# Kernel tuning notes

Measured on AMD Instinct MI355X. Metric: run time of the kernel, lower is better.

Reference implementation:

```python
import jax, jax.numpy as jnp
import numpy as np

N = 10000
E = 80000
NUM_TYPES = 1000
IN_CH = 64
EMB = 128
IN_GNN = EMB + IN_CH - 1  # 191
NUM_GRAPHS = 16
NUM_CLASSES = 2


def _glorot(key, shape):
    fan_in, fan_out = shape[0], shape[1]
    lim = jnp.sqrt(6.0 / (fan_in + fan_out))
    return jax.random.uniform(key, shape, jnp.float32, -lim, lim)


def setup_inputs() -> dict:
    key = jax.random.key(0)
    ks = jax.random.split(key, 20)
    node_type_ids = jax.random.randint(ks[0], (N,), 0, NUM_TYPES)
    other_feats = jax.random.normal(ks[1], (N, IN_CH - 1), jnp.float32)
    edge_index = jax.random.randint(ks[2], (2, E), 0, N)
    batch = jnp.sort(jax.random.randint(ks[3], (N,), 0, NUM_GRAPHS))
    params = dict(
        emb=jax.random.normal(ks[4], (NUM_TYPES, EMB), jnp.float32),
        W1=_glorot(ks[5], (IN_GNN, 2048)), b1=jnp.zeros((2048,), jnp.float32),
        W2=_glorot(ks[6], (2048, 1024)), b2=jnp.zeros((1024,), jnp.float32),
        W3=_glorot(ks[7], (1024, 1024)), b3=jnp.zeros((1024,), jnp.float32),
        h1w=_glorot(ks[8], (1024, 1024)), h1b=jnp.zeros((1024,), jnp.float32),
        h2w=_glorot(ks[9], (1024, 1024)), h2b=jnp.zeros((1024,), jnp.float32),
        h3w=_glorot(ks[10], (1024, 512)), h3b=jnp.zeros((512,), jnp.float32),
        ow=_glorot(ks[11], (512, NUM_CLASSES)), ob=jnp.zeros((NUM_CLASSES,), jnp.float32),
    )
    return dict(node_type_ids=node_type_ids, other_feats=other_feats,
                edge_index=edge_index, batch=batch, **params)


def _gcn_norm(edge_index, num_nodes):
    # add self loops + symmetric normalization D^-1/2 (A+I) D^-1/2 (PyG GCNConv defaults)
    loop = jnp.arange(num_nodes, dtype=edge_index.dtype)
    src = jnp.concatenate([edge_index[0], loop])
    dst = jnp.concatenate([edge_index[1], loop])
    deg = jax.ops.segment_sum(jnp.ones_like(src, jnp.float32), dst, num_segments=num_nodes)
    dinv = jnp.where(deg > 0, jax.lax.rsqrt(jnp.maximum(deg, 1.0)), 0.0)
    norm = dinv[src] * dinv[dst]
    return src, dst, norm


def _gcn_conv(x, src, dst, norm, W, b):
    h = x @ W                                    # [N, out] dense GEMM first (PyG order)
    msg = h[src] * norm[:, None]                 # gather + scale over edges
    agg = jax.ops.segment_sum(msg, dst, num_segments=x.shape[0])  # scatter-add
    return agg + b


def reference(node_type_ids, other_feats, edge_index, batch,
              emb, W1, b1, W2, b2, W3, b3,
              h1w, h1b, h2w, h2b, h3w, h3b, ow, ob):
    # eval mode: dropout is identity
    x = jnp.concatenate([emb[node_type_ids], other_feats], axis=-1)  # [N, 191]
    src, dst, norm = _gcn_norm(edge_index, x.shape[0])
    x = jax.nn.relu(_gcn_conv(x, src, dst, norm, W1, b1))
    x = jax.nn.relu(_gcn_conv(x, src, dst, norm, W2, b2))
    x = jax.nn.relu(_gcn_conv(x, src, dst, norm, W3, b3))
    # global mean pool over graphs
    sums = jax.ops.segment_sum(x, batch, num_segments=NUM_GRAPHS)
    cnts = jax.ops.segment_sum(jnp.ones((x.shape[0],), jnp.float32), batch, num_segments=NUM_GRAPHS)
    g = sums / jnp.maximum(cnts, 1.0)[:, None]   # [G, 1024]
    g = jax.nn.relu(g @ h1w + h1b)
    g = jax.nn.relu(g @ h2w + h2b)
    g = jax.nn.relu(g @ h3w + h3b)
    return g @ ow + ob                           # [G, num_classes]
```

## Files before the change

kernel.cpp:

```cpp
#include <hip/hip_runtime.h>


#define N_NODES 10000
#define N_EDGES 80000
#define EMB_DIM 128
#define FEAT_DIM 63
#define IN_GNN 191
#define IN_STRIDE 192
#define H1 2048
#define H2 1024
#define NGRAPH 16
#define NCLS 2
#define PCHUNK 8

using ushort = unsigned short;
typedef __attribute__((ext_vector_type(8))) short s8b;
typedef __attribute__((ext_vector_type(4))) float f4v;

__device__ __forceinline__ float us2f(ushort u) {
    union { unsigned int i; float f; } v; v.i = ((unsigned int)u) << 16; return v.f;
}
__device__ __forceinline__ ushort f2us(float f) {
    union { unsigned int i; float f; } v; v.f = f;
    unsigned int r = v.i + 0x7FFFu + ((v.i >> 16) & 1u);
    return (ushort)(r >> 16);
}
__device__ __forceinline__ float ldm(const void* p, long i, int md) {
    return (md == 1) ? us2f(((const ushort*)p)[i]) : ((const float*)p)[i];
}

__global__ void GraphV1EmbLarge_73864847556672_kernel() {}

__global__ void k_prep0(int* __restrict__ a, int na, float* __restrict__ b, int nb,
                        const ushort* __restrict__ feats, int* __restrict__ mode) {
    int i = blockIdx.x * 256 + threadIdx.x;
    if (i < na) a[i] = 0;
    if (i < nb) b[i] = 0.f;
    if (blockIdx.x == 0 && threadIdx.x == 0) {
        int sane = 0;
        for (int j = 0; j < 256; j++) {
            ushort u = feats[j];
            int e = (u >> 7) & 0xFF;
            if (u == 0 || (e >= 97 && e <= 157)) sane++;
        }
        *mode = (sane >= 220) ? 1 : 2;
    }
}

__global__ void k_deg_i(const int* __restrict__ dst, int* __restrict__ cnt) {
    int e = blockIdx.x * blockDim.x + threadIdx.x;
    if (e < N_EDGES) atomicAdd(&cnt[dst[e]], 1);
}
__global__ void k_scan(const int* __restrict__ cnt, int* __restrict__ indptr,
                       float* __restrict__ dinv) {
    __shared__ int part[256];
    int t = threadIdx.x;
    int base = t * 40;
    int s = 0;
    for (int i = 0; i < 40; i++) { int idx = base + i; if (idx < N_NODES) s += cnt[idx]; }
    part[t] = s;
    __syncthreads();
    if (t == 0) {
        int run = 0;
        for (int i = 0; i < 256; i++) { int tmp = part[i]; part[i] = run; run += tmp; }
        indptr[N_NODES] = run;
    }
    __syncthreads();
    int run = part[t];
    for (int i = 0; i < 40; i++) {
        int idx = base + i;
        if (idx < N_NODES) {
            indptr[idx] = run; run += cnt[idx];
            dinv[idx] = rsqrtf((float)cnt[idx] + 1.0f);
        }
    }
}
__global__ void k_fill(const int* __restrict__ src, const int* __restrict__ dst,
                       const int* __restrict__ indptr, int* __restrict__ cursor,
                       const float* __restrict__ dinv, int* __restrict__ ecol,
                       float* __restrict__ ewgt, const int* __restrict__ batch,
                       int* __restrict__ starts) {
    int b = blockIdx.x;
    if (b < 313) {
        int e = b * 256 + threadIdx.x;
        if (e >= N_EDGES) return;
        int d = dst[e], s = src[e];
        int slot = indptr[d] + atomicAdd(&cursor[d], 1);
        ecol[slot] = s;
        ewgt[slot] = dinv[s] * dinv[d];
    } else {
        int i = (b - 313) * 256 + threadIdx.x;
        if (i > N_NODES) return;
        int bc = (i < N_NODES) ? batch[i] : NGRAPH;
        int bp = (i == 0) ? -1 : batch[i - 1];
        for (int g = bp + 1; g <= bc; g++) starts[g] = i;
    }
}

__device__ __forceinline__ void cvt_tile(const void* W, int K, int N, int Kp,
                                         ushort* Wt, int n0, int k0, int md) {
    __shared__ float tile[32][33];
    int tx = threadIdx.x, ty = threadIdx.y;
    for (int r = ty; r < 32; r += 8) {
        int k = k0 + r;
        tile[r][tx] = (k < K) ? ldm(W, (long)k * N + n0 + tx, md) : 0.f;
    }
    __syncthreads();
    for (int r = ty; r < 32; r += 8) {
        int nn = n0 + r, kk = k0 + tx;
        if (kk < Kp) Wt[(long)nn * Kp + kk] = f2us(tile[tx][r]);
    }
}

__global__ void k_cvt_all(const void* W1, const void* W2, const void* W3,
                          const void* h1, const void* h2, const void* h3,
                          ushort* W1t, ushort* W2t, ushort* W3t,
                          ushort* h1t, ushort* h2t, ushort* h3t,
                          const int* __restrict__ types, const void* emb,
                          const void* feats, ushort* __restrict__ x0,
                          const void* b1, const void* b2, const void* b3,
                          float* __restrict__ b1f, float* __restrict__ b2f,
                          float* __restrict__ b3f, const int* __restrict__ mode) {
    int md = *mode;
    int b = blockIdx.x;
    if (b < 384) {
        int t = b;        cvt_tile(W1, IN_GNN, H1, IN_STRIDE, W1t, (t % 64) * 32, (t / 64) * 32, md);
    } else if (b < 2432) {
        int t = b - 384;  cvt_tile(W2, H1, H2, H1, W2t, (t % 32) * 32, (t / 32) * 32, md);
    } else if (b < 3456) {
        int t = b - 2432; cvt_tile(W3, H2, H2, H2, W3t, (t % 32) * 32, (t / 32) * 32, md);
    } else if (b < 4480) {
        int t = b - 3456; cvt_tile(h1, H2, H2, H2, h1t, (t % 32) * 32, (t / 32) * 32, md);
    } else if (b < 5504) {
        int t = b - 4480; cvt_tile(h2, H2, H2, H2, h2t, (t % 32) * 32, (t / 32) * 32, md);
    } else if (b < 6016) {
        int t = b - 5504; cvt_tile(h3, H2, 512, H2, h3t, (t % 16) * 32, (t / 16) * 32, md);
    } else if (b < 16016) {
        int i = b - 6016;
        int c = threadIdx.y * 32 + threadIdx.x;
        if (c >= IN_STRIDE) return;
        float v = 0.f;
        if (c < EMB_DIM) v = ldm(emb, (long)types[i] * EMB_DIM + c, md);
        else if (c < IN_GNN) v = ldm(feats, (long)i * FEAT_DIM + (c - EMB_DIM), md);
        x0[(long)i * IN_STRIDE + c] = f2us(v);
    } else {
        int i = (b - 16016) * 256 + threadIdx.y * 32 + threadIdx.x;
        if (i < 2048) b1f[i] = ldm(b1, i, md);
        else if (i < 3072) b2f[i - 2048] = ldm(b2, (long)(i - 2048), md);
        else if (i < 4096) b3f[i - 3072] = ldm(b3, (long)(i - 3072), md);
    }
}

__global__ void k_gather192(const ushort* __restrict__ H, const int* __restrict__ indptr,
                            const int* __restrict__ ecol, const float* __restrict__ ewgt,
                            const float* __restrict__ dinv, ushort* __restrict__ X) {
    int d = blockIdx.x;
    int c = threadIdx.x;
    float ds = dinv[d];
    float acc = us2f(H[(long)d * IN_STRIDE + c]) * ds * ds;
    int s0 = indptr[d], s1 = indptr[d + 1];
    int s = s0;
    for (; s + 1 < s1; s += 2) {
        int sa = ecol[s], sb = ecol[s + 1];
        float wa = ewgt[s], wb = ewgt[s + 1];
        float fa = us2f(H[(long)sa * IN_STRIDE + c]);
        float fb = us2f(H[(long)sb * IN_STRIDE + c]);
        acc += fa * wa + fb * wb;
    }
    if (s < s1) acc += us2f(H[(long)ecol[s] * IN_STRIDE + c]) * ewgt[s];
    X[(long)d * IN_STRIDE + c] = f2us(acc);
}

__global__ __launch_bounds__(64) void k_gather_slice(
    const ushort* __restrict__ H, const int* __restrict__ indptr,
    const int* __restrict__ ecol, const float* __restrict__ ewgt,
    const float* __restrict__ dinv, const float* __restrict__ bias,
    ushort* __restrict__ X) {
    int L = blockIdx.x;
    int d = L >> 3;
    int c2 = (L & 7) * 128 + threadIdx.x * 2;
    float ds = dinv[d];
    float w0 = ds * ds;
    unsigned int u = *(const unsigned int*)&H[(long)d * H2 + c2];
    float a0 = us2f((ushort)(u & 0xffff)) * w0;
    float a1 = us2f((ushort)(u >> 16)) * w0;
    int s0 = indptr[d], s1 = indptr[d + 1];
    int s = s0;
    for (; s + 1 < s1; s += 2) {
        int sa = ecol[s], sb = ecol[s + 1];
        float wa = ewgt[s], wb = ewgt[s + 1];
        unsigned int ua = *(const unsigned int*)&H[(long)sa * H2 + c2];
        unsigned int ub = *(const unsigned int*)&H[(long)sb * H2 + c2];
        a0 += us2f((ushort)(ua & 0xffff)) * wa + us2f((ushort)(ub & 0xffff)) * wb;
        a1 += us2f((ushort)(ua >> 16)) * wa + us2f((ushort)(ub >> 16)) * wb;
    }
    if (s < s1) {
        unsigned int ua = *(const unsigned int*)&H[(long)ecol[s] * H2 + c2];
        float wa = ewgt[s];
        a0 += us2f((ushort)(ua & 0xffff)) * wa;
        a1 += us2f((ushort)(ua >> 16)) * wa;
    }
    unsigned int o = (unsigned int)f2us(fmaxf(a0 + bias[c2], 0.f))
                   | ((unsigned int)f2us(fmaxf(a1 + bias[c2 + 1], 0.f)) << 16);
    *(unsigned int*)&X[(long)d * H2 + c2] = o;
}

__global__ __launch_bounds__(256) void k_mfma_gemm(
    const ushort* __restrict__ A, int lda, int M,
    const ushort* __restrict__ Wt, int K, int N,
    const float* __restrict__ bias, int relu,
    ushort* __restrict__ C, int NB) {
    __shared__ ushort As[2][128 * 32];
    __shared__ ushort Bs[2][128 * 32];
    int L = blockIdx.x;
    int i = L >> 3;
    int m_t = (L & 7) + (i / NB) * 8;
    int n_t = i % NB;
    int m0 = m_t * 128, n0 = n_t * 128;
    if (m0 >= M) return;
    int tid = threadIdx.x;
    int wave = tid >> 6, lane = tid & 63;
    int wm = (wave & 1) * 64, wn = (wave >> 1) * 64;
    int quad = lane >> 4, l16 = lane & 15;
    int srow = tid >> 2;
    int scol = (tid & 3) * 8;
    int swz = ((srow >> 1) & 3) << 3;
    int rwz = ((l16 >> 1) & 3) << 3;
    int wa0 = srow * 32 + (scol ^ swz);
    int wa1 = (64 + srow) * 32 + (scol ^ swz);

    f4v acc[4][4];
#pragma unroll
    for (int ii = 0; ii < 4; ii++)
#pragma unroll
        for (int jj = 0; jj < 4; jj++) acc[ii][jj] = (f4v)(0.f);

    int gm1 = m0 + srow;       if (gm1 >= M) gm1 = M - 1;
    int gm2 = m0 + 64 + srow;  if (gm2 >= M) gm2 = M - 1;
    const ushort* pa1 = A + (long)gm1 * lda + scol;
    const ushort* pa2 = A + (long)gm2 * lda + scol;
    const ushort* pb1 = Wt + (long)(n0 + srow) * K + scol;
    const ushort* pb2 = Wt + (long)(n0 + 64 + srow) * K + scol;

    int niter = K >> 5;
    s8b va1 = *(const s8b*)pa1;
    s8b va2 = *(const s8b*)pa2;
    s8b vb1 = *(const s8b*)pb1;
    s8b vb2 = *(const s8b*)pb2;
    *(s8b*)&As[0][wa0] = va1;
    *(s8b*)&As[0][wa1] = va2;
    *(s8b*)&Bs[0][wa0] = vb1;
    *(s8b*)&Bs[0][wa1] = vb2;
    if (niter > 1) {
        pa1 += 32; pa2 += 32; pb1 += 32; pb2 += 32;
        va1 = *(const s8b*)pa1;
        va2 = *(const s8b*)pa2;
        vb1 = *(const s8b*)pb1;
        vb2 = *(const s8b*)pb2;
    }

    for (int it = 0; it < niter; it++) {
        int cur = it & 1;
        __syncthreads();
        if (it + 1 < niter) {
            int nxt = cur ^ 1;
            *(s8b*)&As[nxt][wa0] = va1;
            *(s8b*)&As[nxt][wa1] = va2;
            *(s8b*)&Bs[nxt][wa0] = vb1;
            *(s8b*)&Bs[nxt][wa1] = vb2;
            if (it + 2 < niter) {
                pa1 += 32; pa2 += 32; pb1 += 32; pb2 += 32;
                va1 = *(const s8b*)pa1;
                va2 = *(const s8b*)pa2;
                vb1 = *(const s8b*)pb1;
                vb2 = *(const s8b*)pb2;
            }
        }
        s8b a[4], b[4];
#pragma unroll
        for (int ii = 0; ii < 4; ii++)
            a[ii] = *(const s8b*)&As[cur][(wm + ii * 16 + l16) * 32 + (quad * 8 ^ rwz)];
#pragma unroll
        for (int jj = 0; jj < 4; jj++)
            b[jj] = *(const s8b*)&Bs[cur][(wn + jj * 16 + l16) * 32 + (quad * 8 ^ rwz)];
#pragma unroll
        for (int ii = 0; ii < 4; ii++)
#pragma unroll
            for (int jj = 0; jj < 4; jj++)
                acc[ii][jj] = __builtin_amdgcn_mfma_f32_16x16x32_bf16(a[ii], b[jj], acc[ii][jj], 0, 0, 0);
    }

#pragma unroll
    for (int ii = 0; ii < 4; ii++) {
        int row0 = m0 + wm + ii * 16 + quad * 4;
#pragma unroll
        for (int jj = 0; jj < 4; jj++) {
            int colc = n0 + wn + jj * 16 + l16;
            float bv = bias ? bias[colc] : 0.f;
#pragma unroll
            for (int r = 0; r < 4; r++) {
                int row = row0 + r;
                if (row < M) {
                    float v = acc[ii][jj][r] + bv;
                    if (relu) v = fmaxf(v, 0.f);
                    C[(long)row * N + colc] = f2us(v);
                }
            }
        }
    }
}

__global__ void k_pool_part(const ushort* __restrict__ x, const int* __restrict__ starts,
                            float* __restrict__ acc) {
    int g = blockIdx.x / PCHUNK, ch = blockIdx.x % PCHUNK;
    int c = blockIdx.y * 256 + threadIdx.x;
    int s0 = starts[g], s1 = starts[g + 1];
    int len = s1 - s0;
    int per = (len + PCHUNK - 1) / PCHUNK;
    int r0 = s0 + ch * per;
    int r1 = r0 + per; if (r1 > s1) r1 = s1;
    if (r0 >= r1) return;
    float sum = 0.f;
    for (int i = r0; i < r1; i++) sum += us2f(x[(long)i * H2 + c]);
    atomicAdd(&acc[g * H2 + c], sum);
}

__global__ __launch_bounds__(256) void k_head_full(const ushort* __restrict__ A,
                                                   const ushort* __restrict__ Wt,
                                                   const void* __restrict__ bias,
                                                   ushort* __restrict__ out, int N,
                                                   const int* __restrict__ mode) {
    __shared__ float red[4][16][16];
    int md = *mode;
    int n0 = blockIdx.x * 16;
    int wave = threadIdx.x >> 6, lane = threadIdx.x & 63;
    int l16 = lane & 15, quad = lane >> 4;
    int kbase = wave * 256;
    f4v acc = (f4v)(0.f);
#pragma unroll
    for (int kk = 0; kk < 256; kk += 32) {
        int k = kbase + kk + quad * 8;
        s8b a = *(const s8b*)&A[l16 * 1024 + k];
        s8b b = *(const s8b*)&Wt[(long)(n0 + l16) * 1024 + k];
        acc = __builtin_amdgcn_mfma_f32_16x16x32_bf16(a, b, acc, 0, 0, 0);
    }
#pragma unroll
    for (int r = 0; r < 4; r++) red[wave][quad * 4 + r][l16] = acc[r];
    __syncthreads();
    int row = threadIdx.x >> 4, col = threadIdx.x & 15;
    float s = red[0][row][col] + red[1][row][col] + red[2][row][col] + red[3][row][col];
    s = fmaxf(s + ldm(bias, (long)(n0 + col), md), 0.f);
    out[(long)row * N + n0 + col] = f2us(s);
}

__global__ __launch_bounds__(256) void k_head_full_pool(const float* __restrict__ pacc,
                                                        const int* __restrict__ starts,
                                                        const ushort* __restrict__ Wt,
                                                        const void* __restrict__ bias,
                                                        ushort* __restrict__ out, int N,
                                                        const int* __restrict__ mode) {
    __shared__ float red[4][16][16];
    int md = *mode;
    int n0 = blockIdx.x * 16;
    int wave = threadIdx.x >> 6, lane = threadIdx.x & 63;
    int l16 = lane & 15, quad = lane >> 4;
    int cnt = starts[l16 + 1] - starts[l16];
    float rc = 1.f / (float)(cnt > 0 ? cnt : 1);
    int kbase = wave * 256;
    f4v acc = (f4v)(0.f);
#pragma unroll
    for (int kk = 0; kk < 256; kk += 32) {
        int k = kbase + kk + quad * 8;
        s8b a;
        short* ap = (short*)&a;
#pragma unroll
        for (int j = 0; j < 8; j++) ap[j] = (short)f2us(pacc[l16 * 1024 + k + j] * rc);
        s8b b = *(const s8b*)&Wt[(long)(n0 + l16) * 1024 + k];
        acc = __builtin_amdgcn_mfma_f32_16x16x32_bf16(a, b, acc, 0, 0, 0);
    }
#pragma unroll
    for (int r = 0; r < 4; r++) red[wave][quad * 4 + r][l16] = acc[r];
    __syncthreads();
    int row = threadIdx.x >> 4, col = threadIdx.x & 15;
    float s = red[0][row][col] + red[1][row][col] + red[2][row][col] + red[3][row][col];
    s = fmaxf(s + ldm(bias, (long)(n0 + col), md), 0.f);
    out[(long)row * N + n0 + col] = f2us(s);
}

__global__ void k_head_out(const ushort* __restrict__ in, const void* __restrict__ W,
                           const void* __restrict__ b, void* __restrict__ out,
                           const int* __restrict__ mode) {
    int md = *mode;
    int row = blockIdx.x >> 1, cls = blockIdx.x & 1;
    int lane = threadIdx.x;
    float acc = 0.f;
    for (int k = lane; k < 512; k += 64)
        acc += us2f(in[row * 512 + k]) * ldm(W, (long)k * NCLS + cls, md);
#pragma unroll
    for (int off = 32; off > 0; off >>= 1) acc += __shfl_down(acc, off);
    if (lane == 0) {
        float v = acc + ldm(b, (long)cls, md);
        if (md == 1) ((ushort*)out)[row * NCLS + cls] = f2us(v);
        else ((float*)out)[row * NCLS + cls] = v;
    }
}

extern "C" void kernel_launch(void* const* d_in, const int* in_sizes, int n_in,
                              void* d_out, int out_size, void* d_ws, size_t ws_size,
                              hipStream_t stream) {
    static const int EXPECT[19] = {
        10000, 630000, 160000, 10000, 128000,
        391168, 2048, 2097152, 1024, 1048576, 1024,
        1048576, 1024, 1048576, 1024, 524288, 512, 1024, 2
    };
    if (n_in != 19) { hipMemsetAsync(d_out, 0x48, 64, stream); return; }
    for (int i = 0; i < 19; i++)
        if (in_sizes[i] != EXPECT[i]) { hipMemsetAsync(d_out, 0x50 + i, 64, stream); return; }
    if (ws_size < (size_t)90000000) { hipMemsetAsync(d_out, 0x49, 64, stream); return; }

    const int* node_types = (const int*)d_in[0];
    const void* other = d_in[1];
    const int* e_src = (const int*)d_in[2];
    const int* e_dst = e_src + N_EDGES;
    const int* batch = (const int*)d_in[3];

    char* w = (char*)d_ws;
    int* mode = (int*)w;      w += 256;
    int* cnt = (int*)w;       w += 10240 * 4;
    int* cursor = (int*)w;    w += 10240 * 4;
    float* dinv = (float*)w;  w += 10240 * 4;
    int* starts = (int*)w;    w += 256;
    int* indptr = (int*)w;    w += 10240 * 4;
    int* ecol = (int*)w;      w += 81920 * 4;
    float* ewgt = (float*)w;  w += 81920 * 4;
    float* b1f = (float*)w;   w += 2048 * 4;
    float* b2f = (float*)w;   w += 1024 * 4;
    float* b3f = (float*)w;   w += 1024 * 4;
    float* pacc = (float*)w;  w += 16 * 1024 * 4;
    ushort* hA = (ushort*)w;  w += 16 * 1024 * 2;
    ushort* hB = (ushort*)w;  w += 16 * 1024 * 2;
    ushort* x0 = (ushort*)w;  w += 1920000 * 2;
    ushort* A1 = (ushort*)w;  w += 1920000 * 2;
    ushort* W1t = (ushort*)w; w += 393216 * 2;
    ushort* W2t = (ushort*)w; w += 2097152 * 2;
    ushort* W3t = (ushort*)w; w += 1048576 * 2;
    ushort* h1wt = (ushort*)w; w += 1048576 * 2;
    ushort* h2wt = (ushort*)w; w += 1048576 * 2;
    ushort* h3wt = (ushort*)w; w += 524288 * 2;
    ushort* Hb = (ushort*)w;  w += 20480000 * 2;
    ushort* Gb = (ushort*)w;  w += 10240000 * 2;
    ushort* x2 = Hb;
    ushort* x3 = Hb + (size_t)N_NODES * H2;

    hipGetLastError();
    k_prep0<<<80, 256, 0, stream>>>(cnt, 20480, pacc, NGRAPH * H2, (const ushort*)other, mode);
    hipError_t e0 = hipGetLastError();
    if (e0 != hipSuccess) { hipMemsetAsync(d_out, 0x46, 64, stream); return; }
    k_deg_i<<<(N_EDGES + 255) / 256, 256, 0, stream>>>(e_dst, cnt);
    k_scan<<<1, 256, 0, stream>>>(cnt, indptr, dinv);
    k_fill<<<313 + 40, 256, 0, stream>>>(e_src, e_dst, indptr, cursor, dinv, ecol, ewgt, batch, starts);

    k_cvt_all<<<16032, dim3(32, 8), 0, stream>>>(d_in[5], d_in[7], d_in[9], d_in[11], d_in[13], d_in[15],
                                                 W1t, W2t, W3t, h1wt, h2wt, h3wt,
                                                 node_types, d_in[4], other, x0,
                                                 d_in[6], d_in[8], d_in[10], b1f, b2f, b3f, mode);

    k_gather192<<<N_NODES, IN_STRIDE, 0, stream>>>(x0, indptr, ecol, ewgt, dinv, A1);
    k_mfma_gemm<<<16 * 80, 256, 0, stream>>>(A1, IN_STRIDE, N_NODES, W1t, IN_STRIDE, H1, b1f, 1, Hb, 16);

    k_mfma_gemm<<<8 * 80, 256, 0, stream>>>(Hb, H1, N_NODES, W2t, H1, H2, nullptr, 0, Gb, 8);
    k_gather_slice<<<N_NODES * 8, 64, 0, stream>>>(Gb, indptr, ecol, ewgt, dinv, b2f, x2);

    k_mfma_gemm<<<8 * 80, 256, 0, stream>>>(x2, H2, N_NODES, W3t, H2, H2, nullptr, 0, Gb, 8);
    k_gather_slice<<<N_NODES * 8, 64, 0, stream>>>(Gb, indptr, ecol, ewgt, dinv, b3f, x3);

    k_pool_part<<<dim3(NGRAPH * PCHUNK, H2 / 256), 256, 0, stream>>>(x3, starts, pacc);

    k_head_full_pool<<<64, 256, 0, stream>>>(pacc, starts, h1wt, d_in[12], hA, 1024, mode);
    k_head_full<<<64, 256, 0, stream>>>(hA, h2wt, d_in[14], hB, 1024, mode);
    k_head_full<<<32, 256, 0, stream>>>(hB, h3wt, d_in[16], hA, 512, mode);
    k_head_out<<<NGRAPH * NCLS, 64, 0, stream>>>(hA, d_in[17], d_in[18], d_out, mode);

    hipError_t e1 = hipGetLastError();
    if (e1 != hipSuccess) hipMemsetAsync(d_out, 0x47, 64, stream);
}
```

Baseline: 399.8 us.

## Split-K layer 2/3 GEMMs and fold partial sums into a wider vectorized gather

Layers 2 and 3 now run their GEMMs split-K in two halves over a second grid dimension, writing two bf16 partial outputs. This doubles the block count (640 to 1280) for better CU occupancy. The gather kernel is rewritten to one block per node with 128 threads. Each thread reads 16-byte vectors from both partials, sums them, and applies the edge weights with a 4-edge unrolled loop. The cost is twice the partial-output traffic in the gather, extra bf16 rounding of the partials, and a larger workspace.

```diff
diff --git a/kernel.cpp b/kernel.cpp
--- a/kernel.cpp
+++ b/kernel.cpp
@@ -171,47 +171,87 @@
     X[(long)d * IN_STRIDE + c] = f2us(acc);
 }
 
-__global__ __launch_bounds__(64) void k_gather_slice(
-    const ushort* __restrict__ H, const int* __restrict__ indptr,
-    const int* __restrict__ ecol, const float* __restrict__ ewgt,
-    const float* __restrict__ dinv, const float* __restrict__ bias,
-    ushort* __restrict__ X) {
-    int L = blockIdx.x;
-    int d = L >> 3;
-    int c2 = (L & 7) * 128 + threadIdx.x * 2;
+__device__ __forceinline__ void unpack8(uint4 u, float* f) {
+    f[0] = us2f((ushort)(u.x & 0xffff)); f[1] = us2f((ushort)(u.x >> 16));
+    f[2] = us2f((ushort)(u.y & 0xffff)); f[3] = us2f((ushort)(u.y >> 16));
+    f[4] = us2f((ushort)(u.z & 0xffff)); f[5] = us2f((ushort)(u.z >> 16));
+    f[6] = us2f((ushort)(u.w & 0xffff)); f[7] = us2f((ushort)(u.w >> 16));
+}
+
+__global__ void k_gather2(const ushort* __restrict__ H, const int* __restrict__ indptr,
+                          const int* __restrict__ ecol, const float* __restrict__ ewgt,
+                          const float* __restrict__ dinv, const float* __restrict__ bias,
+                          ushort* __restrict__ X) {
+    const long SOFF = (long)N_NODES * H2;
+    int d = blockIdx.x;
+    int c8 = threadIdx.x * 8;
     float ds = dinv[d];
-    float w0 = ds * ds;
-    unsigned int u = *(const unsigned int*)&H[(long)d * H2 + c2];
-    float a0 = us2f((ushort)(u & 0xffff)) * w0;
-    float a1 = us2f((ushort)(u >> 16)) * w0;
+    float a[8], f0[8], f1[8];
+    {
+        uint4 u1 = *(const uint4*)&H[(long)d * H2 + c8];
+        uint4 u2 = *(const uint4*)&H[SOFF + (long)d * H2 + c8];
+        unpack8(u1, f0);
+        unpack8(u2, f1);
+        float w0 = ds * ds;
+#pragma unroll
+        for (int r = 0; r < 8; r++) a[r] = (f0[r] + f1[r]) * w0;
+    }
     int s0 = indptr[d], s1 = indptr[d + 1];
     int s = s0;
-    for (; s + 1 < s1; s += 2) {
-        int sa = ecol[s], sb = ecol[s + 1];
-        float wa = ewgt[s], wb = ewgt[s + 1];
-        unsigned int ua = *(const unsigned int*)&H[(long)sa * H2 + c2];
-        unsigned int ub = *(const unsigned int*)&H[(long)sb * H2 + c2];
-        a0 += us2f((ushort)(ua & 0xffff)) * wa + us2f((ushort)(ub & 0xffff)) * wb;
-        a1 += us2f((ushort)(ua >> 16)) * wa + us2f((ushort)(ub >> 16)) * wb;
-    }
-    if (s < s1) {
-        unsigned int ua = *(const unsigned int*)&H[(long)ecol[s] * H2 + c2];
-        float wa = ewgt[s];
-        a0 += us2f((ushort)(ua & 0xffff)) * wa;
-        a1 += us2f((ushort)(ua >> 16)) * wa;
-    }
-    unsigned int o = (unsigned int)f2us(fmaxf(a0 + bias[c2], 0.f))
-                   | ((unsigned int)f2us(fmaxf(a1 + bias[c2 + 1], 0.f)) << 16);
-    *(unsigned int*)&X[(long)d * H2 + c2] = o;
+    for (; s + 3 < s1; s += 4) {
+        int sc[4];
+        float wv[4];
+        uint4 u[8];
+#pragma unroll
+        for (int q = 0; q < 4; q++) { sc[q] = ecol[s + q]; wv[q] = ewgt[s + q]; }
+#pragma unroll
+        for (int q = 0; q < 4; q++) {
+            u[2 * q] = *(const uint4*)&H[(long)sc[q] * H2 + c8];
+            u[2 * q + 1] = *(const uint4*)&H[SOFF + (long)sc[q] * H2 + c8];
+        }
+#pragma unroll
+        for (int q = 0; q < 4; q++) {
+            unpack8(u[2 * q], f0);
+            unpack8(u[2 * q + 1], f1);
+#pragma unroll
+            for (int r = 0; r < 8; r++) a[r] += (f0[r] + f1[r]) * wv[q];
+        }
+    }
+    for (; s < s1; s++) {
+        int sc = ecol[s];
+        float wv = ewgt[s];
+        uint4 u1 = *(const uint4*)&H[(long)sc * H2 + c8];
+        uint4 u2 = *(const uint4*)&H[SOFF + (long)sc * H2 + c8];
+        unpack8(u1, f0);
+        unpack8(u2, f1);
+#pragma unroll
+        for (int r = 0; r < 8; r++) a[r] += (f0[r] + f1[r]) * wv;
+    }
+    uint4 o;
+    unsigned int p0 = (unsigned int)f2us(fmaxf(a[0] + bias[c8 + 0], 0.f));
+    unsigned int p1 = (unsigned int)f2us(fmaxf(a[1] + bias[c8 + 1], 0.f));
+    unsigned int p2 = (unsigned int)f2us(fmaxf(a[2] + bias[c8 + 2], 0.f));
+    unsigned int p3 = (unsigned int)f2us(fmaxf(a[3] + bias[c8 + 3], 0.f));
+    unsigned int p4 = (unsigned int)f2us(fmaxf(a[4] + bias[c8 + 4], 0.f));
+    unsigned int p5 = (unsigned int)f2us(fmaxf(a[5] + bias[c8 + 5], 0.f));
+    unsigned int p6 = (unsigned int)f2us(fmaxf(a[6] + bias[c8 + 6], 0.f));
+    unsigned int p7 = (unsigned int)f2us(fmaxf(a[7] + bias[c8 + 7], 0.f));
+    o.x = p0 | (p1 << 16); o.y = p2 | (p3 << 16);
+    o.z = p4 | (p5 << 16); o.w = p6 | (p7 << 16);
+    *(uint4*)&X[(long)d * H2 + c8] = o;
 }
 
 __global__ __launch_bounds__(256) void k_mfma_gemm(
     const ushort* __restrict__ A, int lda, int M,
-    const ushort* __restrict__ Wt, int K, int N,
+    const ushort* __restrict__ Wt, int ldb, int Ksub, int N,
     const float* __restrict__ bias, int relu,
     ushort* __restrict__ C, int NB) {
     __shared__ ushort As[2][128 * 32];
     __shared__ ushort Bs[2][128 * 32];
+    int split = blockIdx.y;
+    A += (long)split * Ksub;
+    Wt += (long)split * Ksub;
+    C += (long)split * M * N;
     int L = blockIdx.x;
     int i = L >> 3;
     int m_t = (L & 7) + (i / NB) * 8;
@@ -239,10 +279,10 @@
     int gm2 = m0 + 64 + srow;  if (gm2 >= M) gm2 = M - 1;
     const ushort* pa1 = A + (long)gm1 * lda + scol;
     const ushort* pa2 = A + (long)gm2 * lda + scol;
-    const ushort* pb1 = Wt + (long)(n0 + srow) * K + scol;
-    const ushort* pb2 = Wt + (long)(n0 + 64 + srow) * K + scol;
-
-    int niter = K >> 5;
+    const ushort* pb1 = Wt + (long)(n0 + srow) * ldb + scol;
+    const ushort* pb2 = Wt + (long)(n0 + 64 + srow) * ldb + scol;
+
+    int niter = Ksub >> 5;
     s8b va1 = *(const s8b*)pa1;
     s8b va2 = *(const s8b*)pa2;
     s8b vb1 = *(const s8b*)pb1;
@@ -416,7 +456,7 @@
     if (n_in != 19) { hipMemsetAsync(d_out, 0x48, 64, stream); return; }
     for (int i = 0; i < 19; i++)
         if (in_sizes[i] != EXPECT[i]) { hipMemsetAsync(d_out, 0x50 + i, 64, stream); return; }
-    if (ws_size < (size_t)90000000) { hipMemsetAsync(d_out, 0x49, 64, stream); return; }
+    if (ws_size < (size_t)105000000) { hipMemsetAsync(d_out, 0x49, 64, stream); return; }
 
     const int* node_types = (const int*)d_in[0];
     const void* other = d_in[1];
@@ -448,7 +488,7 @@
     ushort* h2wt = (ushort*)w; w += 1048576 * 2;
     ushort* h3wt = (ushort*)w; w += 524288 * 2;
     ushort* Hb = (ushort*)w;  w += 20480000 * 2;
-    ushort* Gb = (ushort*)w;  w += 10240000 * 2;
+    ushort* Gb = (ushort*)w;  w += 2 * 10240000 * 2;
     ushort* x2 = Hb;
     ushort* x3 = Hb + (size_t)N_NODES * H2;
 
@@ -466,13 +506,13 @@
                                                  d_in[6], d_in[8], d_in[10], b1f, b2f, b3f, mode);
 
     k_gather192<<<N_NODES, IN_STRIDE, 0, stream>>>(x0, indptr, ecol, ewgt, dinv, A1);
-    k_mfma_gemm<<<16 * 80, 256, 0, stream>>>(A1, IN_STRIDE, N_NODES, W1t, IN_STRIDE, H1, b1f, 1, Hb, 16);
-
-    k_mfma_gemm<<<8 * 80, 256, 0, stream>>>(Hb, H1, N_NODES, W2t, H1, H2, nullptr, 0, Gb, 8);
-    k_gather_slice<<<N_NODES * 8, 64, 0, stream>>>(Gb, indptr, ecol, ewgt, dinv, b2f, x2);
-
-    k_mfma_gemm<<<8 * 80, 256, 0, stream>>>(x2, H2, N_NODES, W3t, H2, H2, nullptr, 0, Gb, 8);
-    k_gather_slice<<<N_NODES * 8, 64, 0, stream>>>(Gb, indptr, ecol, ewgt, dinv, b3f, x3);
+    k_mfma_gemm<<<dim3(16 * 80, 1), 256, 0, stream>>>(A1, IN_STRIDE, N_NODES, W1t, IN_STRIDE, IN_STRIDE, H1, b1f, 1, Hb, 16);
+
+    k_mfma_gemm<<<dim3(8 * 80, 2), 256, 0, stream>>>(Hb, H1, N_NODES, W2t, H1, H1 / 2, H2, nullptr, 0, Gb, 8);
+    k_gather2<<<N_NODES, 128, 0, stream>>>(Gb, indptr, ecol, ewgt, dinv, b2f, x2);
+
+    k_mfma_gemm<<<dim3(8 * 80, 2), 256, 0, stream>>>(x2, H2, N_NODES, W3t, H2, H2 / 2, H2, nullptr, 0, Gb, 8);
+    k_gather2<<<N_NODES, 128, 0, stream>>>(Gb, indptr, ecol, ewgt, dinv, b3f, x3);
 
     k_pool_part<<<dim3(NGRAPH * PCHUNK, H2 / 256), 256, 0, stream>>>(x3, starts, pacc);
 
```

New measurement: 459.6 us. 15.0% more time.
